# Optimization experiments

Hardware: AMD Instinct MI355X
Metric: run time of the kernel (lower is better)

Reference implementation:

```python
import jax, jax.numpy as jnp
import numpy as np

D_IN = 4097   # 4096 obj feat + 1 depth
D_H1 = 512
D_H2 = 256
N_HEADS = 4
D_HEAD = D_H2 // N_HEADS
D_FF = 512


def setup_inputs() -> dict:
    key = jax.random.key(0)
    ks = jax.random.split(key, 20)
    B, T, N = 2, 100, 30
    s = lambda *sh: 1.0 / np.sqrt(sh[0])
    inp = {
        "object_features": jax.random.normal(ks[0], (B, T, N, 4096), jnp.float32),
        "object_depths": jax.random.uniform(ks[1], (B, T, N, 1), jnp.float32),
        # spatial encoder (2-layer fully-connected message passing)
        "W1a": jax.random.normal(ks[2], (D_IN, D_H1), jnp.float32) * s(D_IN),
        "W2a": jax.random.normal(ks[3], (D_IN, D_H1), jnp.float32) * s(D_IN),
        "b1a": jnp.zeros((D_H1,), jnp.float32),
        "W1b": jax.random.normal(ks[4], (D_H1, D_H2), jnp.float32) * s(D_H1),
        "W2b": jax.random.normal(ks[5], (D_H1, D_H2), jnp.float32) * s(D_H1),
        "b1b": jnp.zeros((D_H2,), jnp.float32),
        # temporal transformer encoder layer (post-LN)
        "Wq": jax.random.normal(ks[6], (D_H2, D_H2), jnp.float32) * s(D_H2),
        "Wk": jax.random.normal(ks[7], (D_H2, D_H2), jnp.float32) * s(D_H2),
        "Wv": jax.random.normal(ks[8], (D_H2, D_H2), jnp.float32) * s(D_H2),
        "Wo": jax.random.normal(ks[9], (D_H2, D_H2), jnp.float32) * s(D_H2),
        "ln1_g": jnp.ones((D_H2,), jnp.float32),
        "ln1_b": jnp.zeros((D_H2,), jnp.float32),
        "Wf1": jax.random.normal(ks[10], (D_H2, D_FF), jnp.float32) * s(D_H2),
        "bf1": jnp.zeros((D_FF,), jnp.float32),
        "Wf2": jax.random.normal(ks[11], (D_FF, D_H2), jnp.float32) * s(D_FF),
        "bf2": jnp.zeros((D_H2,), jnp.float32),
        "ln2_g": jnp.ones((D_H2,), jnp.float32),
        "ln2_b": jnp.zeros((D_H2,), jnp.float32),
        # classifier
        "Wc": jax.random.normal(ks[12], (D_H2, 1), jnp.float32) * s(D_H2),
        "bc": jnp.zeros((1,), jnp.float32),
    }
    return inp


def _layer_norm(x, g, b, eps=1e-5):
    mu = jnp.mean(x, axis=-1, keepdims=True)
    var = jnp.var(x, axis=-1, keepdims=True)
    return (x - mu) * jax.lax.rsqrt(var + eps) * g + b


def _forward(object_features, object_depths, W1a, W2a, b1a, W1b, W2b, b1b,
             Wq, Wk, Wv, Wo, ln1_g, ln1_b, Wf1, bf1, Wf2, bf2, ln2_g, ln2_b,
             Wc, bc):
    B, T, N, _ = object_features.shape
    x = jnp.concatenate([object_features, object_depths], axis=-1)  # (B,T,N,4097)
    # fully-connected graph (torch.combinations, both directions):
    # aggregated message for node i = mean over all j != i.
    def mp(h, Ws, Wn, b):
        neigh = (jnp.sum(h, axis=2, keepdims=True) - h) / (N - 1)
        return jax.nn.relu(h @ Ws + neigh @ Wn + b)
    h = mp(x, W1a, W2a, b1a)      # (B,T,N,512)
    h = mp(h, W1b, W2b, b1b)      # (B,T,N,256)
    g = jnp.mean(h, axis=2)       # global mean pool -> (B,T,256)
    # temporal transformer encoder (self-attention over T, post-LN)
    q = (g @ Wq).reshape(B, T, N_HEADS, D_HEAD)
    k = (g @ Wk).reshape(B, T, N_HEADS, D_HEAD)
    v = (g @ Wv).reshape(B, T, N_HEADS, D_HEAD)
    scores = jnp.einsum("bthd,bshd->bhts", q, k) / np.sqrt(D_HEAD)
    attn = jax.nn.softmax(scores, axis=-1)
    ctx = jnp.einsum("bhts,bshd->bthd", attn, v).reshape(B, T, D_H2) @ Wo
    y = _layer_norm(g + ctx, ln1_g, ln1_b)
    ff = jax.nn.relu(y @ Wf1 + bf1) @ Wf2 + bf2
    z = _layer_norm(y + ff, ln2_g, ln2_b)  # (B,T,256)
    # dropout is identity in eval mode -> probs2 == probs, uncertainty == 0
    logits = (z @ Wc + bc).squeeze(-1)     # (B,T)
    probs = jax.nn.sigmoid(logits)
    uncertainty = jnp.zeros_like(probs)
    return probs, uncertainty


def reference(object_features, object_depths, W1a, W2a, b1a, W1b, W2b, b1b,
              Wq, Wk, Wv, Wo, ln1_g, ln1_b, Wf1, bf1, Wf2, bf2, ln2_g, ln2_b,
              Wc, bc):
    return _forward(object_features, object_depths, W1a, W2a, b1a, W1b, W2b,
                    b1b, Wq, Wk, Wv, Wo, ln1_g, ln1_b, Wf1, bf1, Wf2, bf2,
                    ln2_g, ln2_b, Wc, bc)
```

## Files before the change

### kernel.cpp

```cpp
#include <hip/hip_runtime.h>
#include <hip/hip_bf16.h>
#include <stdint.h>

typedef unsigned short u16;
typedef __attribute__((ext_vector_type(8))) short short8;
typedef __attribute__((ext_vector_type(4))) float floatx4;
typedef __attribute__((ext_vector_type(4))) unsigned short ushort4_t;

#define BT 200
#define NOBJ 30
#define KP2 4224
#define DIN 4097
#define DH1 512
#define DH2 256
#define DFF 512
#define MPAD 6016
#define CHZ 176
#define NBIGW (132*16)
#define NSMALL 512
#define NCONV (BT*3)
#define NZERO 128

__device__ __forceinline__ u16 f2bf(float f) {
    union { float f; uint32_t u; } c; c.f = f;
    uint32_t u = c.u;
    u += 0x7FFF + ((u >> 16) & 1);
    return (u16)(u >> 16);
}

__device__ __forceinline__ void load16_lds(const u16* g, u16* l) {
    __builtin_amdgcn_global_load_lds(
        (const __attribute__((address_space(1))) void*)g,
        (__attribute__((address_space(3))) void*)l, 16, 0, 0);
}

__device__ __forceinline__ size_t tile_off(int ytile, int row, int c8) {
    int z = c8 / CHZ, rem = c8 - z * CHZ;
    int i = rem >> 3, kw = rem & 7;
    int ks = kw ^ (row & 7);
    return ((((size_t)(ytile * 3 + z) * 22 + i) * 128 + row) * 64) + ks * 8;
}

__global__ void prep_all(const float* __restrict__ W1a, const float* __restrict__ W2a,
                         const float* __restrict__ W1b, const float* __restrict__ W2b,
                         const float* __restrict__ feat, const float* __restrict__ depth,
                         u16* __restrict__ Wc1T, u16* __restrict__ W2aTs,
                         u16* __restrict__ Wc2T, u16* __restrict__ W2bTs,
                         u16* __restrict__ XbT, u16* __restrict__ SbT,
                         float* __restrict__ zeroBase, size_t zeroQuads) {
    __shared__ float t1[32][33];
    __shared__ float t2[32][33];
    int bid = blockIdx.x, tid = threadIdx.x;
    if (bid < NBIGW) {
        int kb = (bid % 132) * 32, jb = (bid / 132) * 32;
        int tx = tid & 31, ty = tid >> 5;
        #pragma unroll
        for (int r = 0; r < 32; r += 8) {
            int k = kb + ty + r, j = jb + tx;
            float a = 0.f, b = 0.f;
            if (k < DIN) { a = W1a[k * DH1 + j]; b = W2a[k * DH1 + j]; }
            float bs = b * (1.f / 29.f);
            t1[ty + r][tx] = a - bs;
            t2[ty + r][tx] = bs;
        }
        __syncthreads();
        #pragma unroll
        for (int r = 0; r < 32; r += 8) {
            int j = jb + ty + r, k = kb + tx;
            int x = j >> 7, row = j & 127;
            size_t off = tile_off(x, row, k >> 3) + (k & 7);
            Wc1T[off]  = f2bf(t1[tx][ty + r]);
            W2aTs[off] = f2bf(t2[tx][ty + r]);
        }
    } else if (bid < NBIGW + NSMALL) {
        int idx = (bid - NBIGW) * 256 + tid;
        int j = idx >> 9, k = idx & 511;
        float a = W1b[k * DH2 + j];
        float b = W2b[k * DH2 + j] * (1.f / 29.f);
        Wc2T[j * DH1 + k]  = f2bf(a - b);
        W2bTs[j * DH1 + k] = f2bf(b);
    } else if (bid < NBIGW + NSMALL + NCONV) {
        int cid = bid - NBIGW - NSMALL;
        int bt = cid / 3;
        int c8 = (cid % 3) * 256 + tid;
        if (c8 >= 528) return;
        int k8 = c8 * 8;
        float s[8] = {};
        for (int n = 0; n < NOBJ; n++) {
            int r = bt * NOBJ + n;
            float v[8];
            if (k8 + 7 < 4096) {
                float4 a = *(const float4*)(feat + (size_t)r * 4096 + k8);
                float4 b = *(const float4*)(feat + (size_t)r * 4096 + k8 + 4);
                v[0]=a.x; v[1]=a.y; v[2]=a.z; v[3]=a.w;
                v[4]=b.x; v[5]=b.y; v[6]=b.z; v[7]=b.w;
            } else {
                #pragma unroll
                for (int e = 0; e < 8; e++) v[e] = 0.f;
                if (k8 == 4096) v[0] = depth[r];
            }
            short8 o;
            #pragma unroll
            for (int e = 0; e < 8; e++) { s[e] += v[e]; o[e] = (short)f2bf(v[e]); }
            *(short8*)(XbT + tile_off(r >> 7, r & 127, c8)) = o;
        }
        short8 so;
        #pragma unroll
        for (int e = 0; e < 8; e++) so[e] = (short)f2bf(s[e]);
        *(short8*)(SbT + tile_off(bt >> 7, bt & 127, c8)) = so;
    } else {
        int zid = bid - NBIGW - NSMALL - NCONV;
        float4* p = (float4*)zeroBase;
        float4 zz = {0.f, 0.f, 0.f, 0.f};
        for (size_t idx = (size_t)zid * 256 + tid; idx < zeroQuads; idx += (size_t)NZERO * 256)
            p[idx] = zz;
    }
}

__global__ __launch_bounds__(256) void gemmA(
    const u16* __restrict__ XbT, const u16* __restrict__ WaT,
    const u16* __restrict__ SbT, const u16* __restrict__ WsT,
    float* __restrict__ hacc, float* __restrict__ uOut) {
    __shared__ __align__(16) u16 Al[8192];
    __shared__ __align__(16) u16 Bl[8192];
    int bid = blockIdx.x;
    const u16 *Abase, *Bbase;
    float* outF;
    int m0, n0, M;
    if (bid < 564) {
        int x = bid & 3, y = (bid >> 2) % 47, z = bid / 188;
        Abase = XbT + (size_t)((y * 3 + z) * 22) * 8192;
        Bbase = WaT + (size_t)((x * 3 + z) * 22) * 8192;
        outF = hacc; M = 6000; m0 = y * 128; n0 = x * 128;
    } else {
        int rem = bid - 564;
        int x = rem & 3, y = (rem >> 2) & 1, z = rem >> 3;
        Abase = SbT + (size_t)((y * 3 + z) * 22) * 8192;
        Bbase = WsT + (size_t)((x * 3 + z) * 22) * 8192;
        outF = uOut; M = BT; m0 = y * 128; n0 = x * 128;
    }
    int tid = threadIdx.x, lane = tid & 63, w = tid >> 6;
    floatx4 acc[4][4] = {};
    int lrow = lane & 15, q = lane >> 4;
    int wm = (w & 1) * 64, wn = (w >> 1) * 64;
    int swz = lrow & 7;

    for (int i = 0; i < 22; i++) {
        const u16* as = Abase + (size_t)i * 8192;
        const u16* bs = Bbase + (size_t)i * 8192;
        #pragma unroll
        for (int it = 0; it < 4; it++) {
            load16_lds(as + (it * 256 + tid) * 8, Al + it * 2048 + w * 512);
            load16_lds(bs + (it * 256 + tid) * 8, Bl + it * 2048 + w * 512);
        }
        __syncthreads();
        #pragma unroll
        for (int h = 0; h < 2; h++) {
            int ci = h * 4 + q;
            int so = (ci ^ swz) * 8;
            short8 af[4], bfv[4];
            #pragma unroll
            for (int ii = 0; ii < 4; ii++)
                af[ii] = *(short8*)(Al + (wm + ii * 16 + lrow) * 64 + so);
            #pragma unroll
            for (int j = 0; j < 4; j++)
                bfv[j] = *(short8*)(Bl + (wn + j * 16 + lrow) * 64 + so);
            #pragma unroll
            for (int ii = 0; ii < 4; ii++)
                #pragma unroll
                for (int j = 0; j < 4; j++)
                    acc[ii][j] = __builtin_amdgcn_mfma_f32_16x16x32_bf16(af[ii], bfv[j], acc[ii][j], 0, 0, 0);
        }
        __syncthreads();
    }

    #pragma unroll
    for (int ii = 0; ii < 4; ii++)
        #pragma unroll
        for (int j = 0; j < 4; j++)
            #pragma unroll
            for (int r = 0; r < 4; r++) {
                int row = m0 + wm + ii * 16 + q * 4 + r;
                int col = n0 + wn + j * 16 + lrow;
                if (row < M)
                    atomicAdd(&outF[(size_t)row * DH1 + col], acc[ii][j][r]);
            }
}

__global__ __launch_bounds__(256) void gemmB(
    const u16* __restrict__ hb, const u16* __restrict__ Wc2T,
    const u16* __restrict__ Shb, const u16* __restrict__ W2bTs,
    float* __restrict__ hacc2, float* __restrict__ u2Out) {
    __shared__ __align__(16) u16 Al[64 * 64];
    __shared__ __align__(16) u16 Bl[128 * 64];
    int bid = blockIdx.x;
    const u16 *A, *B;
    float* outF;
    int m0, n0, kbeg, M;
    if (bid < 376) {
        int x = bid & 1, y = (bid >> 1) % 94, z = bid / 188;
        A = hb; B = Wc2T; outF = hacc2; M = 6000;
        m0 = y * 64; n0 = x * 128; kbeg = z * 256;
    } else {
        int rem = bid - 376;
        int x = rem & 1, y = (rem >> 1) & 3, z = rem >> 3;
        A = Shb; B = W2bTs; outF = u2Out; M = BT;
        m0 = y * 64; n0 = x * 128; kbeg = z * 256;
    }
    int kend = kbeg + 256;
    const int N = DH2, K = DH1;
    int tid = threadIdx.x;
    int lane = tid & 63, w = tid >> 6;
    int srow = tid >> 3, kslot = tid & 7;
    floatx4 acc[2][4] = {};
    int lrow = lane & 15, q = lane >> 4;
    int wm = (w & 1) * 32, wn = (w >> 1) * 64;
    int swz = lrow & 7;

    for (int kb = kbeg; kb < kend; kb += 64) {
        #pragma unroll
        for (int it = 0; it < 2; it++) {
            int row = it * 32 + srow;
            int kph = kslot ^ (row & 7);
            load16_lds(A + (size_t)(m0 + row) * K + kb + kph * 8,
                       Al + it * 2048 + w * 512);
        }
        #pragma unroll
        for (int it = 0; it < 4; it++) {
            int row = it * 32 + srow;
            int kph = kslot ^ (row & 7);
            load16_lds(B + (size_t)(n0 + row) * K + kb + kph * 8,
                       Bl + it * 2048 + w * 512);
        }
        __syncthreads();
        #pragma unroll
        for (int h = 0; h < 2; h++) {
            int ci = h * 4 + q;
            int so = (ci ^ swz) * 8;
            short8 af[2], bfv[4];
            #pragma unroll
            for (int i = 0; i < 2; i++)
                af[i] = *(short8*)(Al + (wm + i * 16 + lrow) * 64 + so);
            #pragma unroll
            for (int j = 0; j < 4; j++)
                bfv[j] = *(short8*)(Bl + (wn + j * 16 + lrow) * 64 + so);
            #pragma unroll
            for (int i = 0; i < 2; i++)
                #pragma unroll
                for (int j = 0; j < 4; j++)
                    acc[i][j] = __builtin_amdgcn_mfma_f32_16x16x32_bf16(af[i], bfv[j], acc[i][j], 0, 0, 0);
        }
        __syncthreads();
    }

    #pragma unroll
    for (int i = 0; i < 2; i++)
        #pragma unroll
        for (int j = 0; j < 4; j++)
            #pragma unroll
            for (int r = 0; r < 4; r++) {
                int row = m0 + wm + i * 16 + q * 4 + r;
                int col = n0 + wn + j * 16 + lrow;
                if (row < M)
                    atomicAdd(&outF[(size_t)row * N + col], acc[i][j][r]);
            }
}

__global__ void reduce1(const float* __restrict__ hacc, const float* __restrict__ u,
                        const float* __restrict__ b1a,
                        u16* __restrict__ hb, u16* __restrict__ Shb) {
    __shared__ float sl[128];
    int bt = blockIdx.x, c0 = blockIdx.y * 128;
    int lc = threadIdx.x & 127, rp = threadIdx.x >> 7;
    int col = c0 + lc;
    float ub = u[bt * DH1 + col] + b1a[col];
    float s = 0.f;
    for (int n = rp; n < NOBJ; n += 2) {
        float v = hacc[(size_t)(bt * NOBJ + n) * DH1 + col] + ub;
        v = v > 0.f ? v : 0.f;
        hb[(size_t)(bt * NOBJ + n) * DH1 + col] = f2bf(v);
        s += v;
    }
    if (rp == 0) sl[lc] = s;
    __syncthreads();
    if (rp == 1) Shb[bt * DH1 + col] = f2bf(sl[lc] + s);
}

__global__ void reduce2_qkv(const float* __restrict__ hacc2, const float* __restrict__ u2,
                            const float* __restrict__ b1b,
                            const float* __restrict__ Wq, const float* __restrict__ Wk,
                            const float* __restrict__ Wv,
                            float* __restrict__ g, float* __restrict__ q,
                            float* __restrict__ k, float* __restrict__ v) {
    __shared__ float gl[DH2];
    int bt = blockIdx.x, j = threadIdx.x;
    float ub = u2[bt * DH2 + j] + b1b[j];
    float a = 0.f;
    for (int n = 0; n < NOBJ; n++) {
        float vv = hacc2[(size_t)(bt * NOBJ + n) * DH2 + j] + ub;
        a += vv > 0.f ? vv : 0.f;
    }
    a *= (1.f / 30.f);
    gl[j] = a;
    g[bt * DH2 + j] = a;
    __syncthreads();
    float aq = 0.f, ak = 0.f, av = 0.f;
    for (int kk = 0; kk < DH2; kk++) {
        float x = gl[kk];
        aq += x * Wq[kk * DH2 + j];
        ak += x * Wk[kk * DH2 + j];
        av += x * Wv[kk * DH2 + j];
    }
    q[bt * DH2 + j] = aq;
    k[bt * DH2 + j] = ak;
    v[bt * DH2 + j] = av;
}

__device__ __forceinline__ float block_sum256(float v, volatile float* red) {
    #pragma unroll
    for (int o = 32; o > 0; o >>= 1) v += __shfl_down(v, o);
    int w = threadIdx.x >> 6;
    __syncthreads();
    if ((threadIdx.x & 63) == 0) red[w] = v;
    __syncthreads();
    return red[0] + red[1] + red[2] + red[3];
}

__global__ void attn_head(const float* __restrict__ qg, const float* __restrict__ kg,
                          const float* __restrict__ vg, const float* __restrict__ g,
                          const float* __restrict__ Wo,
                          const float* __restrict__ ln1g, const float* __restrict__ ln1b,
                          const float* __restrict__ Wf1, const float* __restrict__ bf1,
                          const float* __restrict__ Wf2, const float* __restrict__ bf2,
                          const float* __restrict__ ln2g, const float* __restrict__ ln2b,
                          const float* __restrict__ Wc, const float* __restrict__ bc,
                          float* __restrict__ out) {
    __shared__ float ql[DH2];
    __shared__ float scl[4][128];
    __shared__ float ctxl[DH2];
    __shared__ float yl[DH2];
    __shared__ float ffl[DFF];
    __shared__ float red[4];
    int row = blockIdx.x, tid = threadIdx.x;
    int base = (row >= 100) ? 100 : 0;
    ql[tid] = qg[row * DH2 + tid];
    __syncthreads();

    for (int p = tid; p < 512; p += 256) {
        int h = p >> 7, s = p & 127;
        if (s < 100) {
            const float* kr = kg + (size_t)(base + s) * DH2 + h * 64;
            float a = 0.f;
            #pragma unroll 8
            for (int d = 0; d < 64; d++) a += ql[h * 64 + d] * kr[d];
            scl[h][s] = a * 0.125f;
        }
    }
    __syncthreads();

    {
        int w = tid >> 6, lane = tid & 63;
        int s2 = 64 + lane;
        float a  = scl[w][lane];
        float b2 = (s2 < 100) ? scl[w][s2] : -1e30f;
        float m = fmaxf(a, b2);
        #pragma unroll
        for (int o = 32; o > 0; o >>= 1) m = fmaxf(m, __shfl_down(m, o));
        m = __shfl(m, 0);
        float e1 = __expf(a - m);
        float e2 = (s2 < 100) ? __expf(b2 - m) : 0.f;
        float sm = e1 + e2;
        #pragma unroll
        for (int o = 32; o > 0; o >>= 1) sm += __shfl_down(sm, o);
        sm = __shfl(sm, 0);
        float r = 1.f / sm;
        scl[w][lane] = e1 * r;
        if (s2 < 100) scl[w][s2] = e2 * r;
    }
    __syncthreads();

    {
        int h = tid >> 6;
        float o = 0.f;
        for (int s = 0; s < 100; s++)
            o += scl[h][s] * vg[(size_t)(base + s) * DH2 + tid];
        ctxl[tid] = o;
    }
    __syncthreads();

    float o = 0.f;
    for (int kk = 0; kk < DH2; kk++) o += ctxl[kk] * Wo[kk * DH2 + tid];
    float t = g[row * DH2 + tid] + o;
    float mu  = block_sum256(t, red) * (1.f / DH2);
    float ex2 = block_sum256(t * t, red) * (1.f / DH2);
    float y = (t - mu) * rsqrtf(ex2 - mu * mu + 1e-5f) * ln1g[tid] + ln1b[tid];
    yl[tid] = y;
    __syncthreads();
    for (int jj = tid; jj < DFF; jj += 256) {
        float a = bf1[jj];
        for (int kk = 0; kk < DH2; kk++) a += yl[kk] * Wf1[kk * DFF + jj];
        ffl[jj] = a > 0.f ? a : 0.f;
    }
    __syncthreads();
    float o2 = bf2[tid];
    for (int kk = 0; kk < DFF; kk++) o2 += ffl[kk] * Wf2[kk * DH2 + tid];
    float z0 = y + o2;
    float mu2  = block_sum256(z0, red) * (1.f / DH2);
    float ex22 = block_sum256(z0 * z0, red) * (1.f / DH2);
    float z = (z0 - mu2) * rsqrtf(ex22 - mu2 * mu2 + 1e-5f) * ln2g[tid] + ln2b[tid];
    float logit = block_sum256(z * Wc[tid], red) + bc[0];
    if (tid == 0) {
        out[row]      = 1.f / (1.f + __expf(-logit));
        out[BT + row] = 0.f;
    }
}

extern "C" void kernel_launch(void* const* d_in, const int* in_sizes, int n_in,
                              void* d_out, int out_size, void* d_ws, size_t ws_size,
                              hipStream_t stream) {
    const float* feat  = (const float*)d_in[0];
    const float* depth = (const float*)d_in[1];
    const float* W1a = (const float*)d_in[2];
    const float* W2a = (const float*)d_in[3];
    const float* b1a = (const float*)d_in[4];
    const float* W1b = (const float*)d_in[5];
    const float* W2b = (const float*)d_in[6];
    const float* b1b = (const float*)d_in[7];
    const float* Wq  = (const float*)d_in[8];
    const float* Wk  = (const float*)d_in[9];
    const float* Wv  = (const float*)d_in[10];
    const float* Wo  = (const float*)d_in[11];
    const float* ln1g = (const float*)d_in[12];
    const float* ln1b = (const float*)d_in[13];
    const float* Wf1 = (const float*)d_in[14];
    const float* bf1 = (const float*)d_in[15];
    const float* Wf2 = (const float*)d_in[16];
    const float* bf2 = (const float*)d_in[17];
    const float* ln2g = (const float*)d_in[18];
    const float* ln2b = (const float*)d_in[19];
    const float* Wc  = (const float*)d_in[20];
    const float* bc  = (const float*)d_in[21];
    float* out = (float*)d_out;
    char* ws = (char*)d_ws;

    size_t off = 0;
    u16* XbT   = (u16*)(ws + off); off += (size_t)MPAD * KP2 * 2;
    u16* SbT   = (u16*)(ws + off); off += (size_t)256 * KP2 * 2;
    u16* Wc1T  = (u16*)(ws + off); off += (size_t)DH1 * KP2 * 2;
    u16* W2aTs = (u16*)(ws + off); off += (size_t)DH1 * KP2 * 2;
    u16* Wc2T  = (u16*)(ws + off); off += (size_t)DH2 * DH1 * 2;
    u16* W2bTs = (u16*)(ws + off); off += (size_t)DH2 * DH1 * 2;
    u16* Shb   = (u16*)(ws + off); off += (size_t)256 * DH1 * 2;
    char* zBase = ws + off;
    float* hacc  = (float*)(ws + off); off += (size_t)6000 * DH1 * 4;
    float* hacc2 = (float*)(ws + off); off += (size_t)6000 * DH2 * 4;
    float* u     = (float*)(ws + off); off += (size_t)BT * DH1 * 4;
    float* u2    = (float*)(ws + off); off += (size_t)BT * DH2 * 4;
    size_t zeroQuads = (size_t)(ws + off - zBase) / 16;
    u16* hb = XbT;
    float* g = (float*)SbT;
    float* q = g + BT * DH2;
    float* k = q + BT * DH2;
    float* v = k + BT * DH2;

    prep_all<<<NBIGW + NSMALL + NCONV + NZERO, 256, 0, stream>>>(
        W1a, W2a, W1b, W2b, feat, depth,
        Wc1T, W2aTs, Wc2T, W2bTs, XbT, SbT, (float*)zBase, zeroQuads);
    gemmA<<<564 + 24, 256, 0, stream>>>(XbT, Wc1T, SbT, W2aTs, hacc, u);
    reduce1<<<dim3(BT, 4), 256, 0, stream>>>(hacc, u, b1a, hb, Shb);
    gemmB<<<376 + 16, 256, 0, stream>>>(hb, Wc2T, Shb, W2bTs, hacc2, u2);
    reduce2_qkv<<<BT, DH2, 0, stream>>>(hacc2, u2, b1b, Wq, Wk, Wv, g, q, k, v);
    attn_head<<<BT, DH2, 0, stream>>>(q, k, v, g, Wo, ln1g, ln1b, Wf1, bf1,
                                      Wf2, bf2, ln2g, ln2b, Wc, bc, out);
}
```

Baseline: 390.8 us.

## Feed fp32 features directly into GEMM and fold depth column into reduce

Drops the prep pass that converted the whole feature tensor to a tiled bf16 copy. The first GEMM now loads fp32 feature rows, converts them to bf16 in registers and writes them into swizzled LDS, while weights stay on the async global-to-LDS path in a plain row-major layout. The depth column (k=4096) is removed from the large GEMM and added back as a rank-1 term in reduce1, and split-K changes from three chunks to two. The goal is to save the write and re-read of a large intermediate, but the A operand is now loaded synchronously in fp32, which doubles its bytes per tile and adds conversion work inside the GEMM loop.

```diff
diff --git a/kernel.cpp b/kernel.cpp
--- a/kernel.cpp
+++ b/kernel.cpp
@@ -5,20 +5,18 @@
 typedef unsigned short u16;
 typedef __attribute__((ext_vector_type(8))) short short8;
 typedef __attribute__((ext_vector_type(4))) float floatx4;
-typedef __attribute__((ext_vector_type(4))) unsigned short ushort4_t;
+typedef __attribute__((ext_vector_type(4))) unsigned int uint4_t;
 
 #define BT 200
 #define NOBJ 30
-#define KP2 4224
+#define KP 4224
 #define DIN 4097
 #define DH1 512
 #define DH2 256
 #define DFF 512
-#define MPAD 6016
-#define CHZ 176
-#define NBIGW (132*16)
+#define NBIGF 2112
 #define NSMALL 512
-#define NCONV (BT*3)
+#define NSUMS (BT*17)
 #define NZERO 128
 
 __device__ __forceinline__ u16 f2bf(float f) {
@@ -28,17 +26,15 @@
     return (u16)(u >> 16);
 }
 
+__device__ __forceinline__ uint32_t pk2(float a, float b) {
+    __hip_bfloat162 h = __float22bfloat162_rn(make_float2(a, b));
+    uint32_t u; __builtin_memcpy(&u, &h, 4); return u;
+}
+
 __device__ __forceinline__ void load16_lds(const u16* g, u16* l) {
     __builtin_amdgcn_global_load_lds(
         (const __attribute__((address_space(1))) void*)g,
         (__attribute__((address_space(3))) void*)l, 16, 0, 0);
-}
-
-__device__ __forceinline__ size_t tile_off(int ytile, int row, int c8) {
-    int z = c8 / CHZ, rem = c8 - z * CHZ;
-    int i = rem >> 3, kw = rem & 7;
-    int ks = kw ^ (row & 7);
-    return ((((size_t)(ytile * 3 + z) * 22 + i) * 128 + row) * 64) + ks * 8;
 }
 
 __global__ void prep_all(const float* __restrict__ W1a, const float* __restrict__ W2a,
@@ -46,12 +42,12 @@
                          const float* __restrict__ feat, const float* __restrict__ depth,
                          u16* __restrict__ Wc1T, u16* __restrict__ W2aTs,
                          u16* __restrict__ Wc2T, u16* __restrict__ W2bTs,
-                         u16* __restrict__ XbT, u16* __restrict__ SbT,
+                         u16* __restrict__ Sb,
                          float* __restrict__ zeroBase, size_t zeroQuads) {
     __shared__ float t1[32][33];
     __shared__ float t2[32][33];
     int bid = blockIdx.x, tid = threadIdx.x;
-    if (bid < NBIGW) {
+    if (bid < NBIGF) {
         int kb = (bid % 132) * 32, jb = (bid / 132) * 32;
         int tx = tid & 31, ty = tid >> 5;
         #pragma unroll
@@ -67,49 +63,32 @@
         #pragma unroll
         for (int r = 0; r < 32; r += 8) {
             int j = jb + ty + r, k = kb + tx;
-            int x = j >> 7, row = j & 127;
-            size_t off = tile_off(x, row, k >> 3) + (k & 7);
-            Wc1T[off]  = f2bf(t1[tx][ty + r]);
-            W2aTs[off] = f2bf(t2[tx][ty + r]);
-        }
-    } else if (bid < NBIGW + NSMALL) {
-        int idx = (bid - NBIGW) * 256 + tid;
+            Wc1T[(size_t)j * KP + k]  = f2bf(t1[tx][ty + r]);
+            W2aTs[(size_t)j * KP + k] = f2bf(t2[tx][ty + r]);
+        }
+    } else if (bid < NBIGF + NSMALL) {
+        int idx = (bid - NBIGF) * 256 + tid;
         int j = idx >> 9, k = idx & 511;
         float a = W1b[k * DH2 + j];
         float b = W2b[k * DH2 + j] * (1.f / 29.f);
         Wc2T[j * DH1 + k]  = f2bf(a - b);
         W2bTs[j * DH1 + k] = f2bf(b);
-    } else if (bid < NBIGW + NSMALL + NCONV) {
-        int cid = bid - NBIGW - NSMALL;
-        int bt = cid / 3;
-        int c8 = (cid % 3) * 256 + tid;
-        if (c8 >= 528) return;
-        int k8 = c8 * 8;
-        float s[8] = {};
-        for (int n = 0; n < NOBJ; n++) {
-            int r = bt * NOBJ + n;
-            float v[8];
-            if (k8 + 7 < 4096) {
-                float4 a = *(const float4*)(feat + (size_t)r * 4096 + k8);
-                float4 b = *(const float4*)(feat + (size_t)r * 4096 + k8 + 4);
-                v[0]=a.x; v[1]=a.y; v[2]=a.z; v[3]=a.w;
-                v[4]=b.x; v[5]=b.y; v[6]=b.z; v[7]=b.w;
-            } else {
-                #pragma unroll
-                for (int e = 0; e < 8; e++) v[e] = 0.f;
-                if (k8 == 4096) v[0] = depth[r];
-            }
-            short8 o;
-            #pragma unroll
-            for (int e = 0; e < 8; e++) { s[e] += v[e]; o[e] = (short)f2bf(v[e]); }
-            *(short8*)(XbT + tile_off(r >> 7, r & 127, c8)) = o;
-        }
-        short8 so;
-        #pragma unroll
-        for (int e = 0; e < 8; e++) so[e] = (short)f2bf(s[e]);
-        *(short8*)(SbT + tile_off(bt >> 7, bt & 127, c8)) = so;
+    } else if (bid < NBIGF + NSMALL + NSUMS) {
+        int cid = bid - NBIGF - NSMALL;
+        int bt = cid / 17;
+        int k = (cid % 17) * 256 + tid;
+        if (k >= KP) return;
+        float s = 0.f;
+        if (k < 4096) {
+            for (int n = 0; n < NOBJ; n++)
+                s += feat[(size_t)(bt * NOBJ + n) * 4096 + k];
+        } else if (k == 4096) {
+            for (int n = 0; n < NOBJ; n++)
+                s += depth[bt * NOBJ + n];
+        }
+        Sb[(size_t)bt * KP + k] = f2bf(s);
     } else {
-        int zid = bid - NBIGW - NSMALL - NCONV;
+        int zid = bid - NBIGF - NSMALL - NSUMS;
         float4* p = (float4*)zeroBase;
         float4 zz = {0.f, 0.f, 0.f, 0.f};
         for (size_t idx = (size_t)zid * 256 + tid; idx < zeroQuads; idx += (size_t)NZERO * 256)
@@ -118,46 +97,76 @@
 }
 
 __global__ __launch_bounds__(256) void gemmA(
-    const u16* __restrict__ XbT, const u16* __restrict__ WaT,
-    const u16* __restrict__ SbT, const u16* __restrict__ WsT,
+    const float* __restrict__ feat, const u16* __restrict__ Wc1T,
+    const u16* __restrict__ Sb, const u16* __restrict__ W2aTs,
     float* __restrict__ hacc, float* __restrict__ uOut) {
     __shared__ __align__(16) u16 Al[8192];
     __shared__ __align__(16) u16 Bl[8192];
     int bid = blockIdx.x;
-    const u16 *Abase, *Bbase;
+    int seg0 = bid < 376;
+    const u16* Bp;
     float* outF;
-    int m0, n0, M;
-    if (bid < 564) {
+    int m0, n0, kbeg, kiters, M;
+    if (seg0) {
         int x = bid & 3, y = (bid >> 2) % 47, z = bid / 188;
-        Abase = XbT + (size_t)((y * 3 + z) * 22) * 8192;
-        Bbase = WaT + (size_t)((x * 3 + z) * 22) * 8192;
-        outF = hacc; M = 6000; m0 = y * 128; n0 = x * 128;
+        Bp = Wc1T; outF = hacc; M = 6000;
+        m0 = y * 128; n0 = x * 128; kbeg = z * 2048; kiters = 32;
     } else {
-        int rem = bid - 564;
+        int rem = bid - 376;
         int x = rem & 3, y = (rem >> 2) & 1, z = rem >> 3;
-        Abase = SbT + (size_t)((y * 3 + z) * 22) * 8192;
-        Bbase = WsT + (size_t)((x * 3 + z) * 22) * 8192;
-        outF = uOut; M = BT; m0 = y * 128; n0 = x * 128;
+        Bp = W2aTs; outF = uOut; M = BT;
+        m0 = y * 128; n0 = x * 128; kbeg = z * 1408; kiters = 22;
     }
     int tid = threadIdx.x, lane = tid & 63, w = tid >> 6;
     floatx4 acc[4][4] = {};
     int lrow = lane & 15, q = lane >> 4;
     int wm = (w & 1) * 64, wn = (w >> 1) * 64;
     int swz = lrow & 7;
-
-    for (int i = 0; i < 22; i++) {
-        const u16* as = Abase + (size_t)i * 8192;
-        const u16* bs = Bbase + (size_t)i * 8192;
-        #pragma unroll
-        for (int it = 0; it < 4; it++) {
-            load16_lds(as + (it * 256 + tid) * 8, Al + it * 2048 + w * 512);
-            load16_lds(bs + (it * 256 + tid) * 8, Bl + it * 2048 + w * 512);
+    int arow = tid >> 1, asg = tid & 1;
+    int grow = m0 + arow; if (grow > 5999) grow = 5999;
+    const float* asrc0 = feat + (size_t)grow * 4096 + asg * 32;
+    u16* adst0 = Al + arow * 64 + ((asg * 4 + 0) ^ (arow & 7)) * 8;
+    u16* adst1 = Al + arow * 64 + ((asg * 4 + 1) ^ (arow & 7)) * 8;
+    u16* adst2 = Al + arow * 64 + ((asg * 4 + 2) ^ (arow & 7)) * 8;
+    u16* adst3 = Al + arow * 64 + ((asg * 4 + 3) ^ (arow & 7)) * 8;
+    int srB = tid >> 3, ksl = tid & 7;
+
+    for (int i = 0; i < kiters; i++) {
+        int kb = kbeg + i * 64;
+        if (seg0) {
+            const float4* s4 = (const float4*)(asrc0 + kb);
+            float4 f0 = s4[0], f1 = s4[1], f2 = s4[2], f3 = s4[3];
+            float4 f4 = s4[4], f5 = s4[5], f6 = s4[6], f7 = s4[7];
+            uint4_t w0 = {pk2(f0.x,f0.y), pk2(f0.z,f0.w), pk2(f1.x,f1.y), pk2(f1.z,f1.w)};
+            uint4_t w1 = {pk2(f2.x,f2.y), pk2(f2.z,f2.w), pk2(f3.x,f3.y), pk2(f3.z,f3.w)};
+            uint4_t w2 = {pk2(f4.x,f4.y), pk2(f4.z,f4.w), pk2(f5.x,f5.y), pk2(f5.z,f5.w)};
+            uint4_t w3 = {pk2(f6.x,f6.y), pk2(f6.z,f6.w), pk2(f7.x,f7.y), pk2(f7.z,f7.w)};
+            *(uint4_t*)adst0 = w0;
+            *(uint4_t*)adst1 = w1;
+            *(uint4_t*)adst2 = w2;
+            *(uint4_t*)adst3 = w3;
+            #pragma unroll
+            for (int it = 0; it < 4; it++) {
+                int rowb = it * 32 + srB;
+                int kph = ksl ^ (rowb & 7);
+                load16_lds(Bp + (size_t)(n0 + rowb) * KP + kb + kph * 8,
+                           Bl + it * 2048 + w * 512);
+            }
+        } else {
+            #pragma unroll
+            for (int it = 0; it < 4; it++) {
+                int rowb = it * 32 + srB;
+                int kph = ksl ^ (rowb & 7);
+                load16_lds(Sb + (size_t)(m0 + rowb) * KP + kb + kph * 8,
+                           Al + it * 2048 + w * 512);
+                load16_lds(Bp + (size_t)(n0 + rowb) * KP + kb + kph * 8,
+                           Bl + it * 2048 + w * 512);
+            }
         }
         __syncthreads();
         #pragma unroll
         for (int h = 0; h < 2; h++) {
-            int ci = h * 4 + q;
-            int so = (ci ^ swz) * 8;
+            int so = ((h * 4 + q) ^ swz) * 8;
             short8 af[4], bfv[4];
             #pragma unroll
             for (int ii = 0; ii < 4; ii++)
@@ -235,8 +244,7 @@
         __syncthreads();
         #pragma unroll
         for (int h = 0; h < 2; h++) {
-            int ci = h * 4 + q;
-            int so = (ci ^ swz) * 8;
+            int so = ((h * 4 + q) ^ swz) * 8;
             short8 af[2], bfv[4];
             #pragma unroll
             for (int i = 0; i < 2; i++)
@@ -268,15 +276,21 @@
 
 __global__ void reduce1(const float* __restrict__ hacc, const float* __restrict__ u,
                         const float* __restrict__ b1a,
+                        const float* __restrict__ depth,
+                        const float* __restrict__ W1a, const float* __restrict__ W2a,
                         u16* __restrict__ hb, u16* __restrict__ Shb) {
     __shared__ float sl[128];
+    __shared__ float dl[NOBJ];
     int bt = blockIdx.x, c0 = blockIdx.y * 128;
     int lc = threadIdx.x & 127, rp = threadIdx.x >> 7;
     int col = c0 + lc;
+    if (threadIdx.x < NOBJ) dl[threadIdx.x] = depth[bt * NOBJ + threadIdx.x];
     float ub = u[bt * DH1 + col] + b1a[col];
+    float wr = W1a[(size_t)4096 * DH1 + col] - W2a[(size_t)4096 * DH1 + col] * (1.f / 29.f);
+    __syncthreads();
     float s = 0.f;
     for (int n = rp; n < NOBJ; n += 2) {
-        float v = hacc[(size_t)(bt * NOBJ + n) * DH1 + col] + ub;
+        float v = hacc[(size_t)(bt * NOBJ + n) * DH1 + col] + ub + dl[n] * wr;
         v = v > 0.f ? v : 0.f;
         hb[(size_t)(bt * NOBJ + n) * DH1 + col] = f2bf(v);
         s += v;
@@ -444,12 +458,12 @@
     char* ws = (char*)d_ws;
 
     size_t off = 0;
-    u16* XbT   = (u16*)(ws + off); off += (size_t)MPAD * KP2 * 2;
-    u16* SbT   = (u16*)(ws + off); off += (size_t)256 * KP2 * 2;
-    u16* Wc1T  = (u16*)(ws + off); off += (size_t)DH1 * KP2 * 2;
-    u16* W2aTs = (u16*)(ws + off); off += (size_t)DH1 * KP2 * 2;
+    u16* Sb    = (u16*)(ws + off); off += (size_t)256 * KP * 2;
+    u16* Wc1T  = (u16*)(ws + off); off += (size_t)DH1 * KP * 2;
+    u16* W2aTs = (u16*)(ws + off); off += (size_t)DH1 * KP * 2;
     u16* Wc2T  = (u16*)(ws + off); off += (size_t)DH2 * DH1 * 2;
     u16* W2bTs = (u16*)(ws + off); off += (size_t)DH2 * DH1 * 2;
+    u16* hb    = (u16*)(ws + off); off += (size_t)6016 * DH1 * 2;
     u16* Shb   = (u16*)(ws + off); off += (size_t)256 * DH1 * 2;
     char* zBase = ws + off;
     float* hacc  = (float*)(ws + off); off += (size_t)6000 * DH1 * 4;
@@ -457,17 +471,16 @@
     float* u     = (float*)(ws + off); off += (size_t)BT * DH1 * 4;
     float* u2    = (float*)(ws + off); off += (size_t)BT * DH2 * 4;
     size_t zeroQuads = (size_t)(ws + off - zBase) / 16;
-    u16* hb = XbT;
-    float* g = (float*)SbT;
-    float* q = g + BT * DH2;
-    float* k = q + BT * DH2;
-    float* v = k + BT * DH2;
-
-    prep_all<<<NBIGW + NSMALL + NCONV + NZERO, 256, 0, stream>>>(
+    float* g = (float*)(ws + off); off += (size_t)BT * DH2 * 4;
+    float* q = (float*)(ws + off); off += (size_t)BT * DH2 * 4;
+    float* k = (float*)(ws + off); off += (size_t)BT * DH2 * 4;
+    float* v = (float*)(ws + off); off += (size_t)BT * DH2 * 4;
+
+    prep_all<<<NBIGF + NSMALL + NSUMS + NZERO, 256, 0, stream>>>(
         W1a, W2a, W1b, W2b, feat, depth,
-        Wc1T, W2aTs, Wc2T, W2bTs, XbT, SbT, (float*)zBase, zeroQuads);
-    gemmA<<<564 + 24, 256, 0, stream>>>(XbT, Wc1T, SbT, W2aTs, hacc, u);
-    reduce1<<<dim3(BT, 4), 256, 0, stream>>>(hacc, u, b1a, hb, Shb);
+        Wc1T, W2aTs, Wc2T, W2bTs, Sb, (float*)zBase, zeroQuads);
+    gemmA<<<376 + 24, 256, 0, stream>>>(feat, Wc1T, Sb, W2aTs, hacc, u);
+    reduce1<<<dim3(BT, 4), 256, 0, stream>>>(hacc, u, b1a, depth, W1a, W2a, hb, Shb);
     gemmB<<<376 + 16, 256, 0, stream>>>(hb, Wc2T, Shb, W2bTs, hacc2, u2);
     reduce2_qkv<<<BT, DH2, 0, stream>>>(hacc2, u2, b1b, Wq, Wk, Wv, g, q, k, v);
     attn_head<<<BT, DH2, 0, stream>>>(q, k, v, g, Wo, ln1g, ln1b, Wf1, bf1,
```

New measurement: 419.5 us. +7.4%, slower.

## Split object sum, sum-GEMM and second GEMM's K range across more blocks

Applied to the files above, without the earlier changes.

The conversion stage now splits each frame's 30-object loop into 4 slices, giving 4x more blocks, and writes 4 partial object sums into an enlarged SbT buffer. The summed-feature GEMM processes these 4 partial rows per frame and atomically accumulates them into the same output row, which folds the partial sums back together. gemmB halves its K chunk so twice as many blocks run. The aim is more parallelism in the latency-bound conversion and small GEMM stages, at the cost of extra atomics, duplicate sum-GEMM work and a little more bf16 rounding from summing partials separately.

```diff
diff --git a/kernel.cpp b/kernel.cpp
--- a/kernel.cpp
+++ b/kernel.cpp
@@ -5,7 +5,6 @@
 typedef unsigned short u16;
 typedef __attribute__((ext_vector_type(8))) short short8;
 typedef __attribute__((ext_vector_type(4))) float floatx4;
-typedef __attribute__((ext_vector_type(4))) unsigned short ushort4_t;
 
 #define BT 200
 #define NOBJ 30
@@ -18,7 +17,7 @@
 #define CHZ 176
 #define NBIGW (132*16)
 #define NSMALL 512
-#define NCONV (BT*3)
+#define NCONV (BT*12)
 #define NZERO 128
 
 __device__ __forceinline__ u16 f2bf(float f) {
@@ -81,12 +80,14 @@
         W2bTs[j * DH1 + k] = f2bf(b);
     } else if (bid < NBIGW + NSMALL + NCONV) {
         int cid = bid - NBIGW - NSMALL;
-        int bt = cid / 3;
-        int c8 = (cid % 3) * 256 + tid;
+        int slice = cid & 3, part = (cid >> 2) % 3, bt = cid / 12;
+        int c8 = part * 256 + tid;
         if (c8 >= 528) return;
+        const int nsA[4] = {0, 8, 16, 23};
+        const int neA[4] = {8, 16, 23, 30};
         int k8 = c8 * 8;
         float s[8] = {};
-        for (int n = 0; n < NOBJ; n++) {
+        for (int n = nsA[slice]; n < neA[slice]; n++) {
             int r = bt * NOBJ + n;
             float v[8];
             if (k8 + 7 < 4096) {
@@ -107,7 +108,8 @@
         short8 so;
         #pragma unroll
         for (int e = 0; e < 8; e++) so[e] = (short)f2bf(s[e]);
-        *(short8*)(SbT + tile_off(bt >> 7, bt & 127, c8)) = so;
+        int grow = slice * 256 + bt;
+        *(short8*)(SbT + tile_off(grow >> 7, grow & 127, c8)) = so;
     } else {
         int zid = bid - NBIGW - NSMALL - NCONV;
         float4* p = (float4*)zeroBase;
@@ -126,18 +128,18 @@
     int bid = blockIdx.x;
     const u16 *Abase, *Bbase;
     float* outF;
-    int m0, n0, M;
-    if (bid < 564) {
+    int m0, n0, seg0 = bid < 564;
+    if (seg0) {
         int x = bid & 3, y = (bid >> 2) % 47, z = bid / 188;
         Abase = XbT + (size_t)((y * 3 + z) * 22) * 8192;
         Bbase = WaT + (size_t)((x * 3 + z) * 22) * 8192;
-        outF = hacc; M = 6000; m0 = y * 128; n0 = x * 128;
+        outF = hacc; m0 = y * 128; n0 = x * 128;
     } else {
         int rem = bid - 564;
-        int x = rem & 3, y = (rem >> 2) & 1, z = rem >> 3;
+        int x = rem & 3, y = (rem >> 2) & 7, z = rem >> 5;
         Abase = SbT + (size_t)((y * 3 + z) * 22) * 8192;
         Bbase = WsT + (size_t)((x * 3 + z) * 22) * 8192;
-        outF = uOut; M = BT; m0 = y * 128; n0 = x * 128;
+        outF = uOut; m0 = y * 128; n0 = x * 128;
     }
     int tid = threadIdx.x, lane = tid & 63, w = tid >> 6;
     floatx4 acc[4][4] = {};
@@ -156,8 +158,7 @@
         __syncthreads();
         #pragma unroll
         for (int h = 0; h < 2; h++) {
-            int ci = h * 4 + q;
-            int so = (ci ^ swz) * 8;
+            int so = ((h * 4 + q) ^ swz) * 8;
             short8 af[4], bfv[4];
             #pragma unroll
             for (int ii = 0; ii < 4; ii++)
@@ -182,8 +183,14 @@
             for (int r = 0; r < 4; r++) {
                 int row = m0 + wm + ii * 16 + q * 4 + r;
                 int col = n0 + wn + j * 16 + lrow;
-                if (row < M)
-                    atomicAdd(&outF[(size_t)row * DH1 + col], acc[ii][j][r]);
+                if (seg0) {
+                    if (row < 6000)
+                        atomicAdd(&outF[(size_t)row * DH1 + col], acc[ii][j][r]);
+                } else {
+                    int urow = row & 255;
+                    if (urow < BT)
+                        atomicAdd(&outF[(size_t)urow * DH1 + col], acc[ii][j][r]);
+                }
             }
 }
 
@@ -197,17 +204,17 @@
     const u16 *A, *B;
     float* outF;
     int m0, n0, kbeg, M;
-    if (bid < 376) {
+    if (bid < 752) {
         int x = bid & 1, y = (bid >> 1) % 94, z = bid / 188;
         A = hb; B = Wc2T; outF = hacc2; M = 6000;
-        m0 = y * 64; n0 = x * 128; kbeg = z * 256;
+        m0 = y * 64; n0 = x * 128; kbeg = z * 128;
     } else {
-        int rem = bid - 376;
+        int rem = bid - 752;
         int x = rem & 1, y = (rem >> 1) & 3, z = rem >> 3;
         A = Shb; B = W2bTs; outF = u2Out; M = BT;
-        m0 = y * 64; n0 = x * 128; kbeg = z * 256;
-    }
-    int kend = kbeg + 256;
+        m0 = y * 64; n0 = x * 128; kbeg = z * 128;
+    }
+    int kend = kbeg + 128;
     const int N = DH2, K = DH1;
     int tid = threadIdx.x;
     int lane = tid & 63, w = tid >> 6;
@@ -235,8 +242,7 @@
         __syncthreads();
         #pragma unroll
         for (int h = 0; h < 2; h++) {
-            int ci = h * 4 + q;
-            int so = (ci ^ swz) * 8;
+            int so = ((h * 4 + q) ^ swz) * 8;
             short8 af[2], bfv[4];
             #pragma unroll
             for (int i = 0; i < 2; i++)
@@ -445,7 +451,7 @@
 
     size_t off = 0;
     u16* XbT   = (u16*)(ws + off); off += (size_t)MPAD * KP2 * 2;
-    u16* SbT   = (u16*)(ws + off); off += (size_t)256 * KP2 * 2;
+    u16* SbT   = (u16*)(ws + off); off += (size_t)1024 * KP2 * 2;
     u16* Wc1T  = (u16*)(ws + off); off += (size_t)DH1 * KP2 * 2;
     u16* W2aTs = (u16*)(ws + off); off += (size_t)DH1 * KP2 * 2;
     u16* Wc2T  = (u16*)(ws + off); off += (size_t)DH2 * DH1 * 2;
@@ -454,8 +460,8 @@
     char* zBase = ws + off;
     float* hacc  = (float*)(ws + off); off += (size_t)6000 * DH1 * 4;
     float* hacc2 = (float*)(ws + off); off += (size_t)6000 * DH2 * 4;
-    float* u     = (float*)(ws + off); off += (size_t)BT * DH1 * 4;
-    float* u2    = (float*)(ws + off); off += (size_t)BT * DH2 * 4;
+    float* u     = (float*)(ws + off); off += (size_t)256 * DH1 * 4;
+    float* u2    = (float*)(ws + off); off += (size_t)256 * DH2 * 4;
     size_t zeroQuads = (size_t)(ws + off - zBase) / 16;
     u16* hb = XbT;
     float* g = (float*)SbT;
@@ -466,9 +472,9 @@
     prep_all<<<NBIGW + NSMALL + NCONV + NZERO, 256, 0, stream>>>(
         W1a, W2a, W1b, W2b, feat, depth,
         Wc1T, W2aTs, Wc2T, W2bTs, XbT, SbT, (float*)zBase, zeroQuads);
-    gemmA<<<564 + 24, 256, 0, stream>>>(XbT, Wc1T, SbT, W2aTs, hacc, u);
+    gemmA<<<564 + 96, 256, 0, stream>>>(XbT, Wc1T, SbT, W2aTs, hacc, u);
     reduce1<<<dim3(BT, 4), 256, 0, stream>>>(hacc, u, b1a, hb, Shb);
-    gemmB<<<376 + 16, 256, 0, stream>>>(hb, Wc2T, Shb, W2bTs, hacc2, u2);
+    gemmB<<<752 + 32, 256, 0, stream>>>(hb, Wc2T, Shb, W2bTs, hacc2, u2);
     reduce2_qkv<<<BT, DH2, 0, stream>>>(hacc2, u2, b1b, Wq, Wk, Wv, g, q, k, v);
     attn_head<<<BT, DH2, 0, stream>>>(q, k, v, g, Wo, ln1g, ln1b, Wf1, bf1,
                                       Wf2, bf2, ln2g, ln2b, Wc, bc, out);
```

After: 393.2 us. No clear change (+0.6%).
